# Performance work log

Hardware: AMD Instinct MI355X
Metric: run time of the kernel (lower is better)

Reference implementation:

```python
import jax, jax.numpy as jnp
import numpy as np

BSZ, SEQ, DIM = 4, 4096, 1024
MEASURE_DIM = 64
TOPK = 16
NUM_TARGETS = 1


def fwht(x):
    """Fast Walsh-Hadamard transform over last dim (power of two), orthonormal scaling."""
    n = x.shape[-1]
    y = x
    h = 1
    while h < n:
        y = y.reshape(*y.shape[:-1], -1, 2, h)
        a, b = y[..., 0, :], y[..., 1, :]
        y = jnp.concatenate((a + b, a - b), axis=-1)
        y = y.reshape(*x.shape[:-1], n)
        h *= 2
    return y * (n ** -0.5)


def setup_inputs() -> dict:
    key = jax.random.key(0)
    kx, kg, ka, kt, ks, kp = jax.random.split(key, 6)
    x = jax.random.normal(kx, (BSZ, SEQ, DIM), dtype=jnp.float32)
    gates = jax.random.uniform(kg, (BSZ, NUM_TARGETS, MEASURE_DIM), dtype=jnp.float32) + 0.5
    alpha = jax.random.uniform(ka, (BSZ, NUM_TARGETS, 1), dtype=jnp.float32) * 0.1
    tau = jax.random.uniform(kt, (BSZ, NUM_TARGETS, 1), dtype=jnp.float32) * 0.02
    signs = jnp.where(jax.random.uniform(ks, (DIM,)) > 0.5, 1.0, -1.0).astype(jnp.float32)
    perm = jax.random.permutation(kp, DIM).astype(jnp.int32)
    inv_perm = jnp.argsort(perm).astype(jnp.int32)
    return {"x": x, "gates": gates, "alpha": alpha, "tau": tau,
            "signs": signs, "perm": perm, "inv_perm": inv_perm, "target_idx": 0}


def reference(x, gates, alpha, tau, signs, perm, inv_perm, target_idx):
    signs_ = signs.astype(x.dtype)
    # ---- sense: sign flip -> permute -> FWHT -> truncate ----
    y = jnp.take((x * signs_[None, None, :]), perm, axis=-1)
    z = fwht(y)[..., :MEASURE_DIM]  # [B, S, m]
    # ---- shrink (topk mode) ----
    gate = gates[:, target_idx][:, None, :]            # [B, 1, m]
    alpha_t = alpha[:, target_idx][:, None, :]         # [B, 1, 1]
    tau_t = jnp.abs(tau[:, target_idx])[:, None, :]    # [B, 1, 1]
    gated = gate * z
    agated = jnp.abs(gated)
    _, idx = jax.lax.top_k(agated, TOPK)               # [B, S, k]
    mask = jax.nn.one_hot(idx, MEASURE_DIM, dtype=gated.dtype).sum(-2)  # [B, S, m]
    sparse = jnp.where((mask > 0) & (agated >= tau_t), gated, jnp.zeros_like(gated))
    zs = alpha_t * sparse
    # ---- reconstruct: pad -> FWHT -> inverse permute -> sign flip ----
    full = jnp.zeros((*zs.shape[:-1], DIM), dtype=zs.dtype).at[..., :MEASURE_DIM].set(zs)
    r = jnp.take(fwht(full), inv_perm, axis=-1) * signs_[None, None, :]
    return x + r
```

## Files before the change

### kernel.cpp

```cpp
#include <hip/hip_runtime.h>

#define SEQ 4096
#define DIM 1024
#define MD 64
#define TOPK 16
#define WPB 2
#define RPW 2
#define RPB (WPB * RPW)

typedef float nfloat4 __attribute__((ext_vector_type(4)));

__global__ __launch_bounds__(WPB * 64) void csa_kernel(
    const float* __restrict__ x,
    const float* __restrict__ gates,
    const float* __restrict__ alpha,
    const float* __restrict__ tau,
    const float* __restrict__ signs,
    const int*   __restrict__ perm,
    const int*   __restrict__ inv_perm,
    const int*   __restrict__ target_idx,
    float*       __restrict__ out)
{
    __shared__ float y[RPB][DIM];

    const int lane = threadIdx.x & 63;
    const int wv   = threadIdx.x >> 6;
    const int r0   = (blockIdx.x * WPB + wv) * RPW;
    const int b    = r0 >> 12;

    float* y0 = y[wv * RPW + 0];
    float* y1 = y[wv * RPW + 1];

    #pragma unroll
    for (int c = 0; c < 4; ++c) {
        const float4 sg = ((const float4*)signs)[c * 64 + lane];
        const float4 xa = ((const float4*)(x + (size_t)(r0 + 0) * DIM))[c * 64 + lane];
        const float4 xb = ((const float4*)(x + (size_t)(r0 + 1) * DIM))[c * 64 + lane];
        float4 a, bq;
        a.x  = xa.x * sg.x; a.y  = xa.y * sg.y; a.z  = xa.z * sg.z; a.w  = xa.w * sg.w;
        bq.x = xb.x * sg.x; bq.y = xb.y * sg.y; bq.z = xb.z * sg.z; bq.w = xb.w * sg.w;
        ((float4*)y0)[c * 64 + lane] = a;
        ((float4*)y1)[c * 64 + lane] = bq;
    }

    float s0 = 0.f, s1 = 0.f;
    #pragma unroll
    for (int k = 0; k < 16; ++k) {
        const int p = perm[lane + 64 * k];
        s0 += y0[p];
        s1 += y1[p];
    }

    float v0 = s0, v1 = s1;
    #pragma unroll
    for (int bit = 1; bit < MD; bit <<= 1) {
        const float o0 = __shfl_xor(v0, bit, 64);
        const float o1 = __shfl_xor(v1, bit, 64);
        v0 = (lane & bit) ? (o0 - v0) : (v0 + o0);
        v1 = (lane & bit) ? (o1 - v1) : (v1 + o1);
    }

    const int   ti   = target_idx[0];
    const float gate = gates[(b + ti) * MD + lane];
    const float tauv = fabsf(tau[b + ti]);
    const float al   = alpha[b + ti];

    const float g0 = gate * v0 * 0.03125f;
    const float g1 = gate * v1 * 0.03125f;
    const float ag0 = fabsf(g0), ag1 = fabsf(g1);

    const unsigned ka0 = __float_as_uint(ag0);
    const unsigned ka1 = __float_as_uint(ag1);
    unsigned T0 = 0u, T1 = 0u;
    #pragma unroll
    for (int bit = 30; bit >= 0; --bit) {
        const unsigned c0 = T0 | (1u << bit);
        const unsigned c1 = T1 | (1u << bit);
        if (__popcll(__ballot(ka0 >= c0)) >= TOPK) T0 = c0;
        if (__popcll(__ballot(ka1 >= c1)) >= TOPK) T1 = c1;
    }
    const int ngt0 = __popcll(__ballot(ka0 > T0));
    const int ngt1 = __popcll(__ballot(ka1 > T1));
    const unsigned long long lm = (1ull << lane) - 1ull;
    const int er0 = __popcll(__ballot(ka0 == T0) & lm);
    const int er1 = __popcll(__ballot(ka1 == T1) & lm);
    const bool k0 = (ka0 > T0) || ((ka0 == T0) && (er0 < TOPK - ngt0));
    const bool k1 = (ka1 > T1) || ((ka1 == T1) && (er1 < TOPK - ngt1));

    float zs0 = (k0 && ag0 >= tauv) ? al * g0 : 0.f;
    float zs1 = (k1 && ag1 >= tauv) ? al * g1 : 0.f;

    #pragma unroll
    for (int bit = 1; bit < MD; bit <<= 1) {
        const float o0 = __shfl_xor(zs0, bit, 64);
        const float o1 = __shfl_xor(zs1, bit, 64);
        zs0 = (lane & bit) ? (o0 - zs0) : (zs0 + o0);
        zs1 = (lane & bit) ? (o1 - zs1) : (zs1 + o1);
    }
    const float w0 = zs0 * 0.03125f;
    const float w1 = zs1 * 0.03125f;

    nfloat4* orow0 = (nfloat4*)(out + (size_t)(r0 + 0) * DIM);
    nfloat4* orow1 = (nfloat4*)(out + (size_t)(r0 + 1) * DIM);
    #pragma unroll
    for (int c = 0; c < 4; ++c) {
        const int4   ip = ((const int4*)inv_perm)[c * 64 + lane];
        const float4 sg = ((const float4*)signs)[c * 64 + lane];
        const float4 t0 = ((const float4*)y0)[c * 64 + lane];
        const float4 t1 = ((const float4*)y1)[c * 64 + lane];
        const float wx0 = __shfl(w0, ip.x & 63, 64);
        const float wy0 = __shfl(w0, ip.y & 63, 64);
        const float wz0 = __shfl(w0, ip.z & 63, 64);
        const float ww0 = __shfl(w0, ip.w & 63, 64);
        const float wx1 = __shfl(w1, ip.x & 63, 64);
        const float wy1 = __shfl(w1, ip.y & 63, 64);
        const float wz1 = __shfl(w1, ip.z & 63, 64);
        const float ww1 = __shfl(w1, ip.w & 63, 64);
        nfloat4 o0, o1;
        o0.x = sg.x * (t0.x + wx0);
        o0.y = sg.y * (t0.y + wy0);
        o0.z = sg.z * (t0.z + wz0);
        o0.w = sg.w * (t0.w + ww0);
        o1.x = sg.x * (t1.x + wx1);
        o1.y = sg.y * (t1.y + wy1);
        o1.z = sg.z * (t1.z + wz1);
        o1.w = sg.w * (t1.w + ww1);
        __builtin_nontemporal_store(o0, &orow0[c * 64 + lane]);
        __builtin_nontemporal_store(o1, &orow1[c * 64 + lane]);
    }
}

extern "C" void kernel_launch(void* const* d_in, const int* in_sizes, int n_in,
                              void* d_out, int out_size, void* d_ws, size_t ws_size,
                              hipStream_t stream) {
    const float* x        = (const float*)d_in[0];
    const float* gates    = (const float*)d_in[1];
    const float* alpha    = (const float*)d_in[2];
    const float* tau      = (const float*)d_in[3];
    const float* signs    = (const float*)d_in[4];
    const int*   perm     = (const int*)d_in[5];
    const int*   inv_perm = (const int*)d_in[6];
    const int*   tgt      = (const int*)d_in[7];
    float*       out      = (float*)d_out;

    const int rows = 4 * SEQ;
    csa_kernel<<<rows / RPB, WPB * 64, 0, stream>>>(x, gates, alpha, tau, signs,
                                                    perm, inv_perm, tgt, out);
}
```

Measured before the change: 123.1 us.

## Loop each wave over two row pairs with register prefetch of next rows

Halves the grid so each block handles two row-pairs in a loop, and keeps perm indices and signs in registers instead of reloading them per row. The next iteration's x rows are loaded into registers while the current rows are in the permute, FWHT, top-k and store phases, overlapping memory latency with compute. It also adds a min-blocks hint to launch_bounds. This raises register pressure (16 perm ints, 4 sign and 8 x float4s) and cuts the number of waves in flight, which may reduce latency hiding.

```diff
diff --git a/kernel.cpp b/kernel.cpp
--- a/kernel.cpp
+++ b/kernel.cpp
@@ -7,10 +7,12 @@
 #define WPB 2
 #define RPW 2
 #define RPB (WPB * RPW)
+#define GRID 2048
+#define ITERS 2
 
 typedef float nfloat4 __attribute__((ext_vector_type(4)));
 
-__global__ __launch_bounds__(WPB * 64) void csa_kernel(
+__global__ __launch_bounds__(WPB * 64, 4) void csa_kernel(
     const float* __restrict__ x,
     const float* __restrict__ gates,
     const float* __restrict__ alpha,
@@ -25,108 +27,134 @@
 
     const int lane = threadIdx.x & 63;
     const int wv   = threadIdx.x >> 6;
-    const int r0   = (blockIdx.x * WPB + wv) * RPW;
-    const int b    = r0 >> 12;
 
     float* y0 = y[wv * RPW + 0];
     float* y1 = y[wv * RPW + 1];
 
+    int pk[16];
+    #pragma unroll
+    for (int k = 0; k < 16; ++k) pk[k] = perm[lane + 64 * k];
+    float4 sg[4];
+    #pragma unroll
+    for (int c = 0; c < 4; ++c) sg[c] = ((const float4*)signs)[c * 64 + lane];
+    const int ti = target_idx[0];
+
+    int r0 = (blockIdx.x * WPB + wv) * RPW;
+    float4 xa[4], xb[4];
     #pragma unroll
     for (int c = 0; c < 4; ++c) {
-        const float4 sg = ((const float4*)signs)[c * 64 + lane];
-        const float4 xa = ((const float4*)(x + (size_t)(r0 + 0) * DIM))[c * 64 + lane];
-        const float4 xb = ((const float4*)(x + (size_t)(r0 + 1) * DIM))[c * 64 + lane];
-        float4 a, bq;
-        a.x  = xa.x * sg.x; a.y  = xa.y * sg.y; a.z  = xa.z * sg.z; a.w  = xa.w * sg.w;
-        bq.x = xb.x * sg.x; bq.y = xb.y * sg.y; bq.z = xb.z * sg.z; bq.w = xb.w * sg.w;
-        ((float4*)y0)[c * 64 + lane] = a;
-        ((float4*)y1)[c * 64 + lane] = bq;
+        xa[c] = ((const float4*)(x + (size_t)(r0 + 0) * DIM))[c * 64 + lane];
+        xb[c] = ((const float4*)(x + (size_t)(r0 + 1) * DIM))[c * 64 + lane];
     }
 
-    float s0 = 0.f, s1 = 0.f;
     #pragma unroll
-    for (int k = 0; k < 16; ++k) {
-        const int p = perm[lane + 64 * k];
-        s0 += y0[p];
-        s1 += y1[p];
-    }
+    for (int t = 0; t < ITERS; ++t) {
+        const int b = r0 >> 12;
 
-    float v0 = s0, v1 = s1;
-    #pragma unroll
-    for (int bit = 1; bit < MD; bit <<= 1) {
-        const float o0 = __shfl_xor(v0, bit, 64);
-        const float o1 = __shfl_xor(v1, bit, 64);
-        v0 = (lane & bit) ? (o0 - v0) : (v0 + o0);
-        v1 = (lane & bit) ? (o1 - v1) : (v1 + o1);
-    }
+        #pragma unroll
+        for (int c = 0; c < 4; ++c) {
+            float4 a, bq;
+            a.x  = xa[c].x * sg[c].x; a.y  = xa[c].y * sg[c].y;
+            a.z  = xa[c].z * sg[c].z; a.w  = xa[c].w * sg[c].w;
+            bq.x = xb[c].x * sg[c].x; bq.y = xb[c].y * sg[c].y;
+            bq.z = xb[c].z * sg[c].z; bq.w = xb[c].w * sg[c].w;
+            ((float4*)y0)[c * 64 + lane] = a;
+            ((float4*)y1)[c * 64 + lane] = bq;
+        }
 
-    const int   ti   = target_idx[0];
-    const float gate = gates[(b + ti) * MD + lane];
-    const float tauv = fabsf(tau[b + ti]);
-    const float al   = alpha[b + ti];
+        const int r0n = r0 + GRID * RPB;
+        if (t + 1 < ITERS) {
+            #pragma unroll
+            for (int c = 0; c < 4; ++c) {
+                xa[c] = ((const float4*)(x + (size_t)(r0n + 0) * DIM))[c * 64 + lane];
+                xb[c] = ((const float4*)(x + (size_t)(r0n + 1) * DIM))[c * 64 + lane];
+            }
+        }
 
-    const float g0 = gate * v0 * 0.03125f;
-    const float g1 = gate * v1 * 0.03125f;
-    const float ag0 = fabsf(g0), ag1 = fabsf(g1);
+        float s0 = 0.f, s1 = 0.f;
+        #pragma unroll
+        for (int k = 0; k < 16; ++k) {
+            s0 += y0[pk[k]];
+            s1 += y1[pk[k]];
+        }
 
-    const unsigned ka0 = __float_as_uint(ag0);
-    const unsigned ka1 = __float_as_uint(ag1);
-    unsigned T0 = 0u, T1 = 0u;
-    #pragma unroll
-    for (int bit = 30; bit >= 0; --bit) {
-        const unsigned c0 = T0 | (1u << bit);
-        const unsigned c1 = T1 | (1u << bit);
-        if (__popcll(__ballot(ka0 >= c0)) >= TOPK) T0 = c0;
-        if (__popcll(__ballot(ka1 >= c1)) >= TOPK) T1 = c1;
-    }
-    const int ngt0 = __popcll(__ballot(ka0 > T0));
-    const int ngt1 = __popcll(__ballot(ka1 > T1));
-    const unsigned long long lm = (1ull << lane) - 1ull;
-    const int er0 = __popcll(__ballot(ka0 == T0) & lm);
-    const int er1 = __popcll(__ballot(ka1 == T1) & lm);
-    const bool k0 = (ka0 > T0) || ((ka0 == T0) && (er0 < TOPK - ngt0));
-    const bool k1 = (ka1 > T1) || ((ka1 == T1) && (er1 < TOPK - ngt1));
+        float v0 = s0, v1 = s1;
+        #pragma unroll
+        for (int bit = 1; bit < MD; bit <<= 1) {
+            const float o0 = __shfl_xor(v0, bit, 64);
+            const float o1 = __shfl_xor(v1, bit, 64);
+            v0 = (lane & bit) ? (o0 - v0) : (v0 + o0);
+            v1 = (lane & bit) ? (o1 - v1) : (v1 + o1);
+        }
 
-    float zs0 = (k0 && ag0 >= tauv) ? al * g0 : 0.f;
-    float zs1 = (k1 && ag1 >= tauv) ? al * g1 : 0.f;
+        const float gate = gates[(b + ti) * MD + lane];
+        const float tauv = fabsf(tau[b + ti]);
+        const float al   = alpha[b + ti];
 
-    #pragma unroll
-    for (int bit = 1; bit < MD; bit <<= 1) {
-        const float o0 = __shfl_xor(zs0, bit, 64);
-        const float o1 = __shfl_xor(zs1, bit, 64);
-        zs0 = (lane & bit) ? (o0 - zs0) : (zs0 + o0);
-        zs1 = (lane & bit) ? (o1 - zs1) : (zs1 + o1);
-    }
-    const float w0 = zs0 * 0.03125f;
-    const float w1 = zs1 * 0.03125f;
+        const float g0 = gate * v0 * 0.03125f;
+        const float g1 = gate * v1 * 0.03125f;
+        const float ag0 = fabsf(g0), ag1 = fabsf(g1);
 
-    nfloat4* orow0 = (nfloat4*)(out + (size_t)(r0 + 0) * DIM);
-    nfloat4* orow1 = (nfloat4*)(out + (size_t)(r0 + 1) * DIM);
-    #pragma unroll
-    for (int c = 0; c < 4; ++c) {
-        const int4   ip = ((const int4*)inv_perm)[c * 64 + lane];
-        const float4 sg = ((const float4*)signs)[c * 64 + lane];
-        const float4 t0 = ((const float4*)y0)[c * 64 + lane];
-        const float4 t1 = ((const float4*)y1)[c * 64 + lane];
-        const float wx0 = __shfl(w0, ip.x & 63, 64);
-        const float wy0 = __shfl(w0, ip.y & 63, 64);
-        const float wz0 = __shfl(w0, ip.z & 63, 64);
-        const float ww0 = __shfl(w0, ip.w & 63, 64);
-        const float wx1 = __shfl(w1, ip.x & 63, 64);
-        const float wy1 = __shfl(w1, ip.y & 63, 64);
-        const float wz1 = __shfl(w1, ip.z & 63, 64);
-        const float ww1 = __shfl(w1, ip.w & 63, 64);
-        nfloat4 o0, o1;
-        o0.x = sg.x * (t0.x + wx0);
-        o0.y = sg.y * (t0.y + wy0);
-        o0.z = sg.z * (t0.z + wz0);
-        o0.w = sg.w * (t0.w + ww0);
-        o1.x = sg.x * (t1.x + wx1);
-        o1.y = sg.y * (t1.y + wy1);
-        o1.z = sg.z * (t1.z + wz1);
-        o1.w = sg.w * (t1.w + ww1);
-        __builtin_nontemporal_store(o0, &orow0[c * 64 + lane]);
-        __builtin_nontemporal_store(o1, &orow1[c * 64 + lane]);
+        const unsigned ka0 = __float_as_uint(ag0);
+        const unsigned ka1 = __float_as_uint(ag1);
+        unsigned T0 = 0u, T1 = 0u;
+        #pragma unroll
+        for (int bit = 30; bit >= 0; --bit) {
+            const unsigned c0 = T0 | (1u << bit);
+            const unsigned c1 = T1 | (1u << bit);
+            if (__popcll(__ballot(ka0 >= c0)) >= TOPK) T0 = c0;
+            if (__popcll(__ballot(ka1 >= c1)) >= TOPK) T1 = c1;
+        }
+        const int ngt0 = __popcll(__ballot(ka0 > T0));
+        const int ngt1 = __popcll(__ballot(ka1 > T1));
+        const unsigned long long lm = (1ull << lane) - 1ull;
+        const int er0 = __popcll(__ballot(ka0 == T0) & lm);
+        const int er1 = __popcll(__ballot(ka1 == T1) & lm);
+        const bool k0 = (ka0 > T0) || ((ka0 == T0) && (er0 < TOPK - ngt0));
+        const bool k1 = (ka1 > T1) || ((ka1 == T1) && (er1 < TOPK - ngt1));
+
+        float zs0 = (k0 && ag0 >= tauv) ? al * g0 : 0.f;
+        float zs1 = (k1 && ag1 >= tauv) ? al * g1 : 0.f;
+
+        #pragma unroll
+        for (int bit = 1; bit < MD; bit <<= 1) {
+            const float o0 = __shfl_xor(zs0, bit, 64);
+            const float o1 = __shfl_xor(zs1, bit, 64);
+            zs0 = (lane & bit) ? (o0 - zs0) : (zs0 + o0);
+            zs1 = (lane & bit) ? (o1 - zs1) : (zs1 + o1);
+        }
+        const float w0 = zs0 * 0.03125f;
+        const float w1 = zs1 * 0.03125f;
+
+        nfloat4* orow0 = (nfloat4*)(out + (size_t)(r0 + 0) * DIM);
+        nfloat4* orow1 = (nfloat4*)(out + (size_t)(r0 + 1) * DIM);
+        #pragma unroll
+        for (int c = 0; c < 4; ++c) {
+            const int4   ip = ((const int4*)inv_perm)[c * 64 + lane];
+            const float4 t0 = ((const float4*)y0)[c * 64 + lane];
+            const float4 t1 = ((const float4*)y1)[c * 64 + lane];
+            const float wx0 = __shfl(w0, ip.x & 63, 64);
+            const float wy0 = __shfl(w0, ip.y & 63, 64);
+            const float wz0 = __shfl(w0, ip.z & 63, 64);
+            const float ww0 = __shfl(w0, ip.w & 63, 64);
+            const float wx1 = __shfl(w1, ip.x & 63, 64);
+            const float wy1 = __shfl(w1, ip.y & 63, 64);
+            const float wz1 = __shfl(w1, ip.z & 63, 64);
+            const float ww1 = __shfl(w1, ip.w & 63, 64);
+            nfloat4 o0, o1;
+            o0.x = sg[c].x * (t0.x + wx0);
+            o0.y = sg[c].y * (t0.y + wy0);
+            o0.z = sg[c].z * (t0.z + wz0);
+            o0.w = sg[c].w * (t0.w + ww0);
+            o1.x = sg[c].x * (t1.x + wx1);
+            o1.y = sg[c].y * (t1.y + wy1);
+            o1.z = sg[c].z * (t1.z + wz1);
+            o1.w = sg[c].w * (t1.w + ww1);
+            __builtin_nontemporal_store(o0, &orow0[c * 64 + lane]);
+            __builtin_nontemporal_store(o1, &orow1[c * 64 + lane]);
+        }
+
+        r0 = r0n;
     }
 }
 
@@ -143,7 +171,6 @@
     const int*   tgt      = (const int*)d_in[7];
     float*       out      = (float*)d_out;
 
-    const int rows = 4 * SEQ;
-    csa_kernel<<<rows / RPB, WPB * 64, 0, stream>>>(x, gates, alpha, tau, signs,
-                                                    perm, inv_perm, tgt, out);
+    csa_kernel<<<GRID, WPB * 64, 0, stream>>>(x, gates, alpha, tau, signs,
+                                              perm, inv_perm, tgt, out);
 }
```

Result: slower. 126.0 us (+2.4%).
